# Optimization experiments

Measured on AMD Instinct MI355X. Metric: run time of the kernel, lower is better.

Reference implementation:

```python
import jax, jax.numpy as jnp
import numpy as np

B, EEG_D, FMRI_D, BD, H, NC = 131072, 128, 64, 128, 4, 2
HD = BD // H  # head dim = 32
EPS = 1e-5

def layernorm(x, g, b):
    m = jnp.mean(x, axis=-1, keepdims=True)
    v = jnp.var(x, axis=-1, keepdims=True)
    return (x - m) * jax.lax.rsqrt(v + EPS) * g + b

def setup_inputs() -> dict:
    key = jax.random.key(0)
    ks = jax.random.split(key, 24)
    r = lambda i, shape, s=0.05: jax.random.normal(ks[i], shape, dtype=jnp.float32) * s
    return {
        'eeg_feats': jax.random.normal(ks[0], (B, EEG_D), dtype=jnp.float32),
        'fmri_feats': jax.random.normal(ks[1], (B, FMRI_D), dtype=jnp.float32),
        # projections (weights stored [in, out])
        'We': r(2, (EEG_D, BD)), 'be': jnp.zeros((BD,)),
        'ge': jnp.ones((BD,)), 'bge': jnp.zeros((BD,)),
        'Wf': r(3, (FMRI_D, BD)), 'bf': jnp.zeros((BD,)),
        'gf': jnp.ones((BD,)), 'bgf': jnp.zeros((BD,)),
        # multihead attention
        'Wq': r(4, (BD, BD)), 'bq': jnp.zeros((BD,)),
        'Wk': r(5, (BD, BD)), 'bk': jnp.zeros((BD,)),
        'Wv': r(6, (BD, BD)), 'bv': jnp.zeros((BD,)),
        'Wo': r(7, (BD, BD)), 'bo': jnp.zeros((BD,)),
        # learned fusion
        'fusion_logits': jnp.zeros((2,)),
        'temperature': jnp.ones(()),
        # classifier
        'Wc1': r(8, (BD, BD // 2)), 'bc1': jnp.zeros((BD // 2,)),
        'gc': jnp.ones((BD // 2,)), 'bgc': jnp.zeros((BD // 2,)),
        'Wc2': r(9, (BD // 2, NC)), 'bc2': jnp.zeros((NC,)),
    }

def reference(eeg_feats, fmri_feats, We, be, ge, bge, Wf, bf, gf, bgf,
              Wq, bq, Wk, bk, Wv, bv, Wo, bo, fusion_logits, temperature,
              Wc1, bc1, gc, bgc, Wc2, bc2):
    # modality projections: Linear + LN + GELU (dropout off at eval)
    eeg_p = jax.nn.gelu(layernorm(eeg_feats @ We + be, ge, bge), approximate=False)
    fmri_p = jax.nn.gelu(layernorm(fmri_feats @ Wf + bf, gf, bgf), approximate=False)

    # cross-attention: query = eeg_p (1 token), kv = [eeg_p, fmri_p] (2 tokens)
    seq = jnp.stack([eeg_p, fmri_p], axis=1)                 # [B, 2, BD]
    q = (eeg_p @ Wq + bq).reshape(B, H, HD)                  # [B, H, HD]
    k = (seq @ Wk + bk).reshape(B, 2, H, HD)
    v = (seq @ Wv + bv).reshape(B, 2, H, HD)
    scores = jnp.einsum('bhd,bkhd->bhk', q, k) / jnp.sqrt(jnp.float32(HD))
    attn = jax.nn.softmax(scores, axis=-1)                   # [B, H, 2]
    ctx = jnp.einsum('bhk,bkhd->bhd', attn, v).reshape(B, BD)
    eeg_enh = ctx @ Wo + bo                                  # [B, BD]

    # learned temperature-scaled fusion over [eeg_enhanced, fmri_proj]
    w = jax.nn.softmax(fusion_logits / temperature, axis=0)
    fused = w[0] * eeg_enh + w[1] * fmri_p                   # [B, BD]

    # classifier: Linear + LN + ReLU + Linear
    h = jax.nn.relu(layernorm(fused @ Wc1 + bc1, gc, bgc))
    logits = h @ Wc2 + bc2                                   # [B, NC]
    return logits
```

## Files before the change

### kernel.cpp

```cpp
#include <hip/hip_runtime.h>
#include <math.h>

#define EPS 1e-5f
#define SCALE 0.17677669529663687f

#define OFF_We  0
#define OFF_Wf  16384
#define OFF_Wq  24576
#define OFF_Wk  40960
#define OFF_Wv  57344
#define OFF_Wo  73728
#define OFF_Wc1 90112
#define PACK_TOTAL 98304

#define CHUNK 8192

typedef __bf16 bf16x8 __attribute__((ext_vector_type(8)));
typedef float f32x4 __attribute__((ext_vector_type(4)));
typedef unsigned short ushort_t;
typedef unsigned short ushortx4 __attribute__((ext_vector_type(4)));

__device__ __forceinline__ ushort_t f2bf(float x) {
    return __builtin_bit_cast(ushort_t, (__bf16)x);
}
__device__ __forceinline__ float bf2f(ushort_t v) {
    unsigned u = ((unsigned)v) << 16;
    return __builtin_bit_cast(float, u);
}

__device__ __forceinline__ ushort_t f2bf_sw(float x) {
    unsigned u = __builtin_bit_cast(unsigned, x);
    u = (u + 0x7fffu + ((u >> 16) & 1u)) >> 16;
    return (ushort_t)u;
}

#define DPPADD(x, ctrl) \
    ((x) + __builtin_bit_cast(float, __builtin_amdgcn_update_dpp( \
        __builtin_bit_cast(int, (x)), __builtin_bit_cast(int, (x)), (ctrl), 0xF, 0xF, false)))

__device__ __forceinline__ float rowsum16(float x) {
    x = DPPADD(x, 0x121);
    x = DPPADD(x, 0x122);
    x = DPPADD(x, 0x124);
    x = DPPADD(x, 0x128);
    return x;
}

__device__ __forceinline__ float gelu_fast(float x) {
    float x2 = x * x;
    float t = fmaf(-0.10294313843f, x2, -2.30220842f);
#if __has_builtin(__builtin_amdgcn_exp2f)
    float e = __builtin_amdgcn_exp2f(x * t);
#else
    float e = __expf(x * t * 0.6931471806f);
#endif
    return x * __builtin_amdgcn_rcpf(1.0f + e);
}

__global__ __launch_bounds__(256) void pack_all(
    const float* __restrict__ We, const float* __restrict__ Wf,
    const float* __restrict__ Wq, const float* __restrict__ Wk,
    const float* __restrict__ Wv, const float* __restrict__ Wo,
    const float* __restrict__ Wc1, ushort_t* __restrict__ ws)
{
    int o = blockIdx.x * 256 + threadIdx.x;
    if (o >= PACK_TOTAL) return;
    const float* W; int K, N, base;
    if (o < OFF_Wf)        { W = We;  K = 128; N = 128; base = OFF_We; }
    else if (o < OFF_Wq)   { W = Wf;  K = 64;  N = 128; base = OFF_Wf; }
    else if (o < OFF_Wk)   { W = Wq;  K = 128; N = 128; base = OFF_Wk == OFF_Wk ? OFF_Wq : OFF_Wq; }
    else if (o < OFF_Wv)   { W = Wk;  K = 128; N = 128; base = OFF_Wk; }
    else if (o < OFF_Wo)   { W = Wv;  K = 128; N = 128; base = OFF_Wv; }
    else if (o < OFF_Wc1)  { W = Wo;  K = 128; N = 128; base = OFF_Wo; }
    else                   { W = Wc1; K = 128; N = 64;  base = OFF_Wc1; }
    int e = o - base;
    int j = e & 7, l = (e >> 3) & 63, rest = e >> 9;
    int KS = K >> 5;
    int s = rest % KS, t = rest / KS;
    int k = s * 32 + ((l >> 4) << 3) + j;
    int n = (t << 4) + (l & 15);
    ws[o] = f2bf_sw(W[k * N + n]);
}

template<int KS>
__device__ __forceinline__ void load_af(bf16x8 af[KS], const ushort_t* A, int lane)
{
    const int quad = lane >> 4, l16 = lane & 15;
    #pragma unroll
    for (int ks = 0; ks < KS; ++ks)
        af[ks] = *(const bf16x8*)(A + l16 * 136 + ks * 32 + quad * 8);
}

template<int KS, int NT4>
__device__ __forceinline__ void mma_c(const bf16x8 af[KS], const ushort_t* sW,
                                      f32x4* acc, int lane)
{
    #pragma unroll
    for (int t = 0; t < NT4; ++t)
        #pragma unroll
        for (int ks = 0; ks < KS; ++ks) {
            bf16x8 bb = *(const bf16x8*)(sW + ((t * KS + ks) * 64 + lane) * 8);
            acc[t] = __builtin_amdgcn_mfma_f32_16x16x32_bf16(af[ks], bb, acc[t], 0, 0, 0);
        }
}

__global__ __launch_bounds__(256, 3) void fusion_stage(
    const float* __restrict__ eeg, const float* __restrict__ fmri,
    const float* __restrict__ be, const float* __restrict__ ge, const float* __restrict__ bge,
    const float* __restrict__ bfb, const float* __restrict__ gf, const float* __restrict__ bgf,
    const float* __restrict__ bq, const float* __restrict__ bk, const float* __restrict__ bv,
    const float* __restrict__ bo,
    const float* __restrict__ fusion_logits, const float* __restrict__ temperature,
    const float* __restrict__ bc1, const float* __restrict__ gc, const float* __restrict__ bgc,
    const float* __restrict__ Wc2, const float* __restrict__ bc2,
    const ushort_t* __restrict__ ws, float* __restrict__ out)
{
    __shared__ __align__(16) ushort_t sW[CHUNK];
    __shared__ __align__(16) ushort_t B1[4][16 * 136];
    __shared__ __align__(16) ushort_t B2[4][16 * 136];

    const int tid = threadIdx.x;
    const int wave = tid >> 6, lane = tid & 63;
    const int quad = lane >> 4, l16 = lane & 15;
    const int rowbase = blockIdx.x * 64 + wave * 16;
    ushort_t* b1 = B1[wave];
    ushort_t* b2 = B2[wave];

    auto stageW = [&](int offU) {
        __syncthreads();
        const char* g = (const char*)(ws + offU) + tid * 16;
        char* l = (char*)sW + tid * 16;
        #pragma unroll
        for (int i = 0; i < 4; ++i)
            __builtin_amdgcn_global_load_lds(
                (const __attribute__((address_space(1))) void*)(g + i * 4096),
                (__attribute__((address_space(3))) void*)(l + i * 4096), 16, 0, 0);
        __syncthreads();
    };

    {
        const float4* src = (const float4*)(eeg + (size_t)rowbase * 128);
        #pragma unroll
        for (int i = 0; i < 8; ++i) {
            int idx = i * 64 + lane;
            float4 v = src[idx];
            int r = idx >> 5, k4 = (idx & 31) * 4;
            *(ushortx4*)&b1[r * 136 + k4] =
                (ushortx4){f2bf(v.x), f2bf(v.y), f2bf(v.z), f2bf(v.w)};
        }
        const float4* srcf = (const float4*)(fmri + (size_t)rowbase * 64);
        #pragma unroll
        for (int i = 0; i < 4; ++i) {
            int idx = i * 64 + lane;
            float4 v = srcf[idx];
            int r = idx >> 4, k4 = (idx & 15) * 4;
            *(ushortx4*)&b2[r * 136 + k4] =
                (ushortx4){f2bf(v.x), f2bf(v.y), f2bf(v.z), f2bf(v.w)};
        }
    }

    float meanS[4], rstdS[4];

    {
        bf16x8 afR[4]; load_af<4>(afR, b1, lane);
        f32x4 acc[8];
        #pragma unroll
        for (int nt = 0; nt < 8; ++nt) {
            float b = be[nt * 16 + l16];
            acc[nt] = (f32x4){b, b, b, b};
        }
        stageW(OFF_We);          mma_c<4, 4>(afR, sW, acc + 0, lane);
        stageW(OFF_We + CHUNK);  mma_c<4, 4>(afR, sW, acc + 4, lane);
        #pragma unroll
        for (int r = 0; r < 4; ++r) {
            float s = 0.f, ss = 0.f;
            #pragma unroll
            for (int nt = 0; nt < 8; ++nt) { float x = acc[nt][r]; s += x; ss = fmaf(x, x, ss); }
            s = rowsum16(s); ss = rowsum16(ss);
            float m = s * (1.f / 128.f);
            meanS[r] = m;
            rstdS[r] = rsqrtf(ss * (1.f / 128.f) - m * m + EPS);
        }
        #pragma unroll
        for (int nt = 0; nt < 8; ++nt) {
            float g = ge[nt * 16 + l16], bb = bge[nt * 16 + l16];
            #pragma unroll
            for (int r = 0; r < 4; ++r) {
                float x = (acc[nt][r] - meanS[r]) * rstdS[r] * g + bb;
                b1[(quad * 4 + r) * 136 + nt * 16 + l16] = f2bf(gelu_fast(x));
            }
        }
    }

    f32x4 fpv[8];
    {
        bf16x8 afR[2]; load_af<2>(afR, b2, lane);
        f32x4 acc[8];
        #pragma unroll
        for (int nt = 0; nt < 8; ++nt) {
            float b = bfb[nt * 16 + l16];
            acc[nt] = (f32x4){b, b, b, b};
        }
        stageW(OFF_Wf);  mma_c<2, 8>(afR, sW, acc, lane);
        #pragma unroll
        for (int r = 0; r < 4; ++r) {
            float s = 0.f, ss = 0.f;
            #pragma unroll
            for (int nt = 0; nt < 8; ++nt) { float x = acc[nt][r]; s += x; ss = fmaf(x, x, ss); }
            s = rowsum16(s); ss = rowsum16(ss);
            float m = s * (1.f / 128.f);
            meanS[r] = m;
            rstdS[r] = rsqrtf(ss * (1.f / 128.f) - m * m + EPS);
        }
        #pragma unroll
        for (int nt = 0; nt < 8; ++nt) {
            float g = gf[nt * 16 + l16], bb = bgf[nt * 16 + l16];
            #pragma unroll
            for (int r = 0; r < 4; ++r) {
                float x = (acc[nt][r] - meanS[r]) * rstdS[r] * g + bb;
                float gv = gelu_fast(x);
                fpv[nt][r] = gv;
                b2[(quad * 4 + r) * 136 + nt * 16 + l16] = f2bf(gv);
            }
        }
    }

    bf16x8 afE[4]; load_af<4>(afE, b1, lane);
    bf16x8 afF[4]; load_af<4>(afF, b2, lane);

    f32x4 q[8];
    {
        #pragma unroll
        for (int nt = 0; nt < 8; ++nt) {
            float b = bq[nt * 16 + l16];
            q[nt] = (f32x4){b, b, b, b};
        }
        stageW(OFF_Wq);          mma_c<4, 4>(afE, sW, q + 0, lane);
        stageW(OFF_Wq + CHUNK);  mma_c<4, 4>(afE, sW, q + 4, lane);
    }

    float a0v[4][4];
    {
        float pd[4][4];
        #pragma unroll
        for (int h = 0; h < 4; ++h)
            #pragma unroll
            for (int r = 0; r < 4; ++r) pd[h][r] = 0.f;
        #pragma unroll
        for (int c = 0; c < 2; ++c) {
            stageW(OFF_Wk + c * CHUNK);
            #pragma unroll
            for (int tl = 0; tl < 4; ++tl) {
                int nt = c * 4 + tl;
                f32x4 e = {0.f, 0.f, 0.f, 0.f}, f = {0.f, 0.f, 0.f, 0.f};
                #pragma unroll
                for (int ks = 0; ks < 4; ++ks) {
                    bf16x8 bb = *(const bf16x8*)(sW + ((tl * 4 + ks) * 64 + lane) * 8);
                    e = __builtin_amdgcn_mfma_f32_16x16x32_bf16(afE[ks], bb, e, 0, 0, 0);
                    f = __builtin_amdgcn_mfma_f32_16x16x32_bf16(afF[ks], bb, f, 0, 0, 0);
                }
                int h = nt >> 1;
                #pragma unroll
                for (int r = 0; r < 4; ++r)
                    pd[h][r] = fmaf(q[nt][r], e[r] - f[r], pd[h][r]);
            }
        }
        #pragma unroll
        for (int h = 0; h < 4; ++h)
            #pragma unroll
            for (int r = 0; r < 4; ++r) {
                float d = rowsum16(pd[h][r]) * SCALE;
                a0v[h][r] = __builtin_amdgcn_rcpf(1.0f + __expf(-d));
            }
    }

    #pragma unroll
    for (int c = 0; c < 2; ++c) {
        stageW(OFF_Wv + c * CHUNK);
        #pragma unroll
        for (int tl = 0; tl < 4; ++tl) {
            int nt = c * 4 + tl;
            float b = bv[nt * 16 + l16];
            f32x4 e = {b, b, b, b}, f = {b, b, b, b};
            #pragma unroll
            for (int ks = 0; ks < 4; ++ks) {
                bf16x8 bb = *(const bf16x8*)(sW + ((tl * 4 + ks) * 64 + lane) * 8);
                e = __builtin_amdgcn_mfma_f32_16x16x32_bf16(afE[ks], bb, e, 0, 0, 0);
                f = __builtin_amdgcn_mfma_f32_16x16x32_bf16(afF[ks], bb, f, 0, 0, 0);
            }
            int h = nt >> 1;
            #pragma unroll
            for (int r = 0; r < 4; ++r) {
                float c0 = fmaf(a0v[h][r], e[r] - f[r], f[r]);
                b1[(quad * 4 + r) * 136 + nt * 16 + l16] = f2bf(c0);
            }
        }
    }

    {
        bf16x8 afC[4]; load_af<4>(afC, b1, lane);
        f32x4 acc[8];
        #pragma unroll
        for (int nt = 0; nt < 8; ++nt) {
            float b = bo[nt * 16 + l16];
            acc[nt] = (f32x4){b, b, b, b};
        }
        stageW(OFF_Wo);          mma_c<4, 4>(afC, sW, acc + 0, lane);
        stageW(OFF_Wo + CHUNK);  mma_c<4, 4>(afC, sW, acc + 4, lane);
        float t = temperature[0];
        float dl = (fusion_logits[0] - fusion_logits[1]) / t;
        float w0 = __builtin_amdgcn_rcpf(1.0f + __expf(-dl));
        float w1 = 1.0f - w0;
        #pragma unroll
        for (int nt = 0; nt < 8; ++nt)
            #pragma unroll
            for (int r = 0; r < 4; ++r) {
                int off = (quad * 4 + r) * 136 + nt * 16 + l16;
                b1[off] = f2bf(w0 * acc[nt][r] + w1 * fpv[nt][r]);
            }
    }

    {
        bf16x8 afU[4]; load_af<4>(afU, b1, lane);
        f32x4 accH[4];
        #pragma unroll
        for (int nt = 0; nt < 4; ++nt) {
            float b = bc1[nt * 16 + l16];
            accH[nt] = (f32x4){b, b, b, b};
        }
        stageW(OFF_Wc1);  mma_c<4, 4>(afU, sW, accH, lane);
        #pragma unroll
        for (int r = 0; r < 4; ++r) {
            float s = 0.f, ss = 0.f;
            #pragma unroll
            for (int nt = 0; nt < 4; ++nt) { float x = accH[nt][r]; s += x; ss = fmaf(x, x, ss); }
            s = rowsum16(s); ss = rowsum16(ss);
            float m = s * (1.f / 64.f);
            meanS[r] = m;
            rstdS[r] = rsqrtf(ss * (1.f / 64.f) - m * m + EPS);
        }
        float hv[4][4];
        #pragma unroll
        for (int nt = 0; nt < 4; ++nt) {
            float g = gc[nt * 16 + l16], bb = bgc[nt * 16 + l16];
            #pragma unroll
            for (int r = 0; r < 4; ++r) {
                float x = (accH[nt][r] - meanS[r]) * rstdS[r] * g + bb;
                hv[nt][r] = fmaxf(x, 0.0f);
            }
        }
        float w2v[4][2];
        #pragma unroll
        for (int nt = 0; nt < 4; ++nt) {
            float2 w = *(const float2*)&Wc2[(nt * 16 + l16) * 2];
            w2v[nt][0] = w.x; w2v[nt][1] = w.y;
        }
        float o0c = bc2[0], o1c = bc2[1];
        #pragma unroll
        for (int r = 0; r < 4; ++r) {
            float p0 = 0.f, p1 = 0.f;
            #pragma unroll
            for (int nt = 0; nt < 4; ++nt) {
                p0 = fmaf(hv[nt][r], w2v[nt][0], p0);
                p1 = fmaf(hv[nt][r], w2v[nt][1], p1);
            }
            p0 = rowsum16(p0); p1 = rowsum16(p1);
            if (l16 == 0) {
                int row = rowbase + quad * 4 + r;
                float2 o; o.x = p0 + o0c; o.y = p1 + o1c;
                *(float2*)&out[row * 2] = o;
            }
        }
    }
}

extern "C" void kernel_launch(void* const* d_in, const int* in_sizes, int n_in,
                              void* d_out, int out_size, void* d_ws, size_t ws_size,
                              hipStream_t stream) {
    const float* eeg  = (const float*)d_in[0];
    const float* fmri = (const float*)d_in[1];
    const float* We   = (const float*)d_in[2];
    const float* be   = (const float*)d_in[3];
    const float* ge   = (const float*)d_in[4];
    const float* bge  = (const float*)d_in[5];
    const float* Wf   = (const float*)d_in[6];
    const float* bf   = (const float*)d_in[7];
    const float* gf   = (const float*)d_in[8];
    const float* bgf  = (const float*)d_in[9];
    const float* Wq   = (const float*)d_in[10];
    const float* bq   = (const float*)d_in[11];
    const float* Wk   = (const float*)d_in[12];
    const float* bk   = (const float*)d_in[13];
    const float* Wv   = (const float*)d_in[14];
    const float* bv   = (const float*)d_in[15];
    const float* Wo   = (const float*)d_in[16];
    const float* bo   = (const float*)d_in[17];
    const float* fl   = (const float*)d_in[18];
    const float* temp = (const float*)d_in[19];
    const float* Wc1  = (const float*)d_in[20];
    const float* bc1  = (const float*)d_in[21];
    const float* gc   = (const float*)d_in[22];
    const float* bgc  = (const float*)d_in[23];
    const float* Wc2  = (const float*)d_in[24];
    const float* bc2  = (const float*)d_in[25];
    float* out = (float*)d_out;
    ushort_t* ws = (ushort_t*)d_ws;

    hipLaunchKernelGGL(pack_all, dim3((PACK_TOTAL + 255) / 256), dim3(256), 0, stream,
                       We, Wf, Wq, Wk, Wv, Wo, Wc1, ws);

    int B = in_sizes[0] / 128;
    int grid = B / 64;
    hipLaunchKernelGGL(fusion_stage, dim3(grid), dim3(256), 0, stream,
                       eeg, fmri, be, ge, bge, bf, gf, bgf,
                       bq, bk, bv, bo, fl, temp, bc1, gc, bgc, Wc2, bc2,
                       ws, out);
}
```

Before: 204.8 us.

## Halve weight staging chunk, XOR-swizzle activation LDS, raise occupancy to 4 blocks

Shrinks the shared weight staging buffer from 8192 to 4096 bf16 elements and removes the row padding (136 to 128) from the per-wave activation buffers, using an XOR swizzle on the column index to avoid bank conflicts. Together these cut LDS per block so launch_bounds can request 4 blocks per CU instead of 3. The cost is twice as many stage/sync rounds per GEMM, each with block-wide barriers and less work between them.

```diff
diff --git a/kernel.cpp b/kernel.cpp
--- a/kernel.cpp
+++ b/kernel.cpp
@@ -13,7 +13,9 @@
 #define OFF_Wc1 90112
 #define PACK_TOTAL 98304
 
-#define CHUNK 8192
+#define CHUNK 4096
+
+#define BOFF(r, c) ((((r) << 7) + (c)) ^ (((r) & 7) << 3))
 
 typedef __bf16 bf16x8 __attribute__((ext_vector_type(8)));
 typedef float f32x4 __attribute__((ext_vector_type(4)));
@@ -68,7 +70,7 @@
     const float* W; int K, N, base;
     if (o < OFF_Wf)        { W = We;  K = 128; N = 128; base = OFF_We; }
     else if (o < OFF_Wq)   { W = Wf;  K = 64;  N = 128; base = OFF_Wf; }
-    else if (o < OFF_Wk)   { W = Wq;  K = 128; N = 128; base = OFF_Wk == OFF_Wk ? OFF_Wq : OFF_Wq; }
+    else if (o < OFF_Wk)   { W = Wq;  K = 128; N = 128; base = OFF_Wq; }
     else if (o < OFF_Wv)   { W = Wk;  K = 128; N = 128; base = OFF_Wk; }
     else if (o < OFF_Wo)   { W = Wv;  K = 128; N = 128; base = OFF_Wv; }
     else if (o < OFF_Wc1)  { W = Wo;  K = 128; N = 128; base = OFF_Wo; }
@@ -88,15 +90,15 @@
     const int quad = lane >> 4, l16 = lane & 15;
     #pragma unroll
     for (int ks = 0; ks < KS; ++ks)
-        af[ks] = *(const bf16x8*)(A + l16 * 136 + ks * 32 + quad * 8);
-}
-
-template<int KS, int NT4>
+        af[ks] = *(const bf16x8*)(A + BOFF(l16, ks * 32 + quad * 8));
+}
+
+template<int KS, int NT>
 __device__ __forceinline__ void mma_c(const bf16x8 af[KS], const ushort_t* sW,
                                       f32x4* acc, int lane)
 {
     #pragma unroll
-    for (int t = 0; t < NT4; ++t)
+    for (int t = 0; t < NT; ++t)
         #pragma unroll
         for (int ks = 0; ks < KS; ++ks) {
             bf16x8 bb = *(const bf16x8*)(sW + ((t * KS + ks) * 64 + lane) * 8);
@@ -104,7 +106,7 @@
         }
 }
 
-__global__ __launch_bounds__(256, 3) void fusion_stage(
+__global__ __launch_bounds__(256, 4) void fusion_stage(
     const float* __restrict__ eeg, const float* __restrict__ fmri,
     const float* __restrict__ be, const float* __restrict__ ge, const float* __restrict__ bge,
     const float* __restrict__ bfb, const float* __restrict__ gf, const float* __restrict__ bgf,
@@ -116,8 +118,8 @@
     const ushort_t* __restrict__ ws, float* __restrict__ out)
 {
     __shared__ __align__(16) ushort_t sW[CHUNK];
-    __shared__ __align__(16) ushort_t B1[4][16 * 136];
-    __shared__ __align__(16) ushort_t B2[4][16 * 136];
+    __shared__ __align__(16) ushort_t B1[4][16 * 128];
+    __shared__ __align__(16) ushort_t B2[4][16 * 128];
 
     const int tid = threadIdx.x;
     const int wave = tid >> 6, lane = tid & 63;
@@ -130,11 +132,12 @@
         __syncthreads();
         const char* g = (const char*)(ws + offU) + tid * 16;
         char* l = (char*)sW + tid * 16;
-        #pragma unroll
-        for (int i = 0; i < 4; ++i)
-            __builtin_amdgcn_global_load_lds(
-                (const __attribute__((address_space(1))) void*)(g + i * 4096),
-                (__attribute__((address_space(3))) void*)(l + i * 4096), 16, 0, 0);
+        __builtin_amdgcn_global_load_lds(
+            (const __attribute__((address_space(1))) void*)g,
+            (__attribute__((address_space(3))) void*)l, 16, 0, 0);
+        __builtin_amdgcn_global_load_lds(
+            (const __attribute__((address_space(1))) void*)(g + 4096),
+            (__attribute__((address_space(3))) void*)(l + 4096), 16, 0, 0);
         __syncthreads();
     };
 
@@ -145,7 +148,7 @@
             int idx = i * 64 + lane;
             float4 v = src[idx];
             int r = idx >> 5, k4 = (idx & 31) * 4;
-            *(ushortx4*)&b1[r * 136 + k4] =
+            *(ushortx4*)&b1[BOFF(r, k4)] =
                 (ushortx4){f2bf(v.x), f2bf(v.y), f2bf(v.z), f2bf(v.w)};
         }
         const float4* srcf = (const float4*)(fmri + (size_t)rowbase * 64);
@@ -154,7 +157,7 @@
             int idx = i * 64 + lane;
             float4 v = srcf[idx];
             int r = idx >> 4, k4 = (idx & 15) * 4;
-            *(ushortx4*)&b2[r * 136 + k4] =
+            *(ushortx4*)&b2[BOFF(r, k4)] =
                 (ushortx4){f2bf(v.x), f2bf(v.y), f2bf(v.z), f2bf(v.w)};
         }
     }
@@ -169,8 +172,11 @@
             float b = be[nt * 16 + l16];
             acc[nt] = (f32x4){b, b, b, b};
         }
-        stageW(OFF_We);          mma_c<4, 4>(afR, sW, acc + 0, lane);
-        stageW(OFF_We + CHUNK);  mma_c<4, 4>(afR, sW, acc + 4, lane);
+        #pragma unroll
+        for (int c = 0; c < 4; ++c) {
+            stageW(OFF_We + c * CHUNK);
+            mma_c<4, 2>(afR, sW, acc + c * 2, lane);
+        }
         #pragma unroll
         for (int r = 0; r < 4; ++r) {
             float s = 0.f, ss = 0.f;
@@ -187,7 +193,7 @@
             #pragma unroll
             for (int r = 0; r < 4; ++r) {
                 float x = (acc[nt][r] - meanS[r]) * rstdS[r] * g + bb;
-                b1[(quad * 4 + r) * 136 + nt * 16 + l16] = f2bf(gelu_fast(x));
+                b1[BOFF(quad * 4 + r, nt * 16 + l16)] = f2bf(gelu_fast(x));
             }
         }
     }
@@ -201,7 +207,8 @@
             float b = bfb[nt * 16 + l16];
             acc[nt] = (f32x4){b, b, b, b};
         }
-        stageW(OFF_Wf);  mma_c<2, 8>(afR, sW, acc, lane);
+        stageW(OFF_Wf);          mma_c<2, 4>(afR, sW, acc + 0, lane);
+        stageW(OFF_Wf + CHUNK);  mma_c<2, 4>(afR, sW, acc + 4, lane);
         #pragma unroll
         for (int r = 0; r < 4; ++r) {
             float s = 0.f, ss = 0.f;
@@ -220,7 +227,7 @@
                 float x = (acc[nt][r] - meanS[r]) * rstdS[r] * g + bb;
                 float gv = gelu_fast(x);
                 fpv[nt][r] = gv;
-                b2[(quad * 4 + r) * 136 + nt * 16 + l16] = f2bf(gv);
+                b2[BOFF(quad * 4 + r, nt * 16 + l16)] = f2bf(gv);
             }
         }
     }
@@ -235,8 +242,11 @@
             float b = bq[nt * 16 + l16];
             q[nt] = (f32x4){b, b, b, b};
         }
-        stageW(OFF_Wq);          mma_c<4, 4>(afE, sW, q + 0, lane);
-        stageW(OFF_Wq + CHUNK);  mma_c<4, 4>(afE, sW, q + 4, lane);
+        #pragma unroll
+        for (int c = 0; c < 4; ++c) {
+            stageW(OFF_Wq + c * CHUNK);
+            mma_c<4, 2>(afE, sW, q + c * 2, lane);
+        }
     }
 
     float a0v[4][4];
@@ -247,11 +257,11 @@
             #pragma unroll
             for (int r = 0; r < 4; ++r) pd[h][r] = 0.f;
         #pragma unroll
-        for (int c = 0; c < 2; ++c) {
+        for (int c = 0; c < 4; ++c) {
             stageW(OFF_Wk + c * CHUNK);
             #pragma unroll
-            for (int tl = 0; tl < 4; ++tl) {
-                int nt = c * 4 + tl;
+            for (int tl = 0; tl < 2; ++tl) {
+                int nt = c * 2 + tl;
                 f32x4 e = {0.f, 0.f, 0.f, 0.f}, f = {0.f, 0.f, 0.f, 0.f};
                 #pragma unroll
                 for (int ks = 0; ks < 4; ++ks) {
@@ -275,11 +285,11 @@
     }
 
     #pragma unroll
-    for (int c = 0; c < 2; ++c) {
+    for (int c = 0; c < 4; ++c) {
         stageW(OFF_Wv + c * CHUNK);
         #pragma unroll
-        for (int tl = 0; tl < 4; ++tl) {
-            int nt = c * 4 + tl;
+        for (int tl = 0; tl < 2; ++tl) {
+            int nt = c * 2 + tl;
             float b = bv[nt * 16 + l16];
             f32x4 e = {b, b, b, b}, f = {b, b, b, b};
             #pragma unroll
@@ -292,7 +302,7 @@
             #pragma unroll
             for (int r = 0; r < 4; ++r) {
                 float c0 = fmaf(a0v[h][r], e[r] - f[r], f[r]);
-                b1[(quad * 4 + r) * 136 + nt * 16 + l16] = f2bf(c0);
+                b1[BOFF(quad * 4 + r, nt * 16 + l16)] = f2bf(c0);
             }
         }
     }
@@ -305,8 +315,11 @@
             float b = bo[nt * 16 + l16];
             acc[nt] = (f32x4){b, b, b, b};
         }
-        stageW(OFF_Wo);          mma_c<4, 4>(afC, sW, acc + 0, lane);
-        stageW(OFF_Wo + CHUNK);  mma_c<4, 4>(afC, sW, acc + 4, lane);
+        #pragma unroll
+        for (int c = 0; c < 4; ++c) {
+            stageW(OFF_Wo + c * CHUNK);
+            mma_c<4, 2>(afC, sW, acc + c * 2, lane);
+        }
         float t = temperature[0];
         float dl = (fusion_logits[0] - fusion_logits[1]) / t;
         float w0 = __builtin_amdgcn_rcpf(1.0f + __expf(-dl));
@@ -314,10 +327,8 @@
         #pragma unroll
         for (int nt = 0; nt < 8; ++nt)
             #pragma unroll
-            for (int r = 0; r < 4; ++r) {
-                int off = (quad * 4 + r) * 136 + nt * 16 + l16;
-                b1[off] = f2bf(w0 * acc[nt][r] + w1 * fpv[nt][r]);
-            }
+            for (int r = 0; r < 4; ++r)
+                b1[BOFF(quad * 4 + r, nt * 16 + l16)] = f2bf(w0 * acc[nt][r] + w1 * fpv[nt][r]);
     }
 
     {
@@ -328,7 +339,8 @@
             float b = bc1[nt * 16 + l16];
             accH[nt] = (f32x4){b, b, b, b};
         }
-        stageW(OFF_Wc1);  mma_c<4, 4>(afU, sW, accH, lane);
+        stageW(OFF_Wc1);          mma_c<4, 2>(afU, sW, accH + 0, lane);
+        stageW(OFF_Wc1 + CHUNK);  mma_c<4, 2>(afU, sW, accH + 2, lane);
         #pragma unroll
         for (int r = 0; r < 4; ++r) {
             float s = 0.f, ss = 0.f;
```

New measurement: 238.5 us. 1.16x slower.
